# Kernel tuning notes

Measured on AMD Instinct MI355X. Metric: run time of the kernel, lower is better.

The kernel has to match this reference:

```python
import jax, jax.numpy as jnp
from jax import lax
import numpy as np

B, M, C, H, W = 32, 2, 256, 16, 16
N = H * W            # 256, square case required by the original bmm chain
DIM = 256            # hardcoded self.dim in the module
THR = 0.1
RATIO = 0.8


def conv2d(x, w, b):
    y = lax.conv_general_dilated(x, w, (1, 1), 'SAME',
                                 dimension_numbers=('NCHW', 'OIHW', 'NCHW'))
    return y + b[None, :, None, None]


def setup_inputs() -> dict:
    key = jax.random.key(0)
    ks = jax.random.split(key, 8)
    return {
        'con_feat': jax.random.normal(ks[0], (B, M, C, H, W), jnp.float32),
        'feat_s':   jax.random.normal(ks[1], (B, M, C, C), jnp.float32),
        'feat_v':   jax.random.uniform(ks[2], (B, M, C), jnp.float32),
        'feat_d':   jax.random.normal(ks[3], (B, M, N, N), jnp.float32),
        'w_enc':    jax.random.normal(ks[4], (C, C, 3, 3), jnp.float32) * 0.02,
        'b_enc':    jnp.zeros((C,), jnp.float32),
        'w_dec':    jax.random.normal(ks[5], (C, C, 3, 3), jnp.float32) * 0.02,
        'b_dec':    jnp.zeros((C,), jnp.float32),
        'w_val':    jax.random.normal(ks[6], (1, 2 * C, 3, 3), jnp.float32) * 0.02,
        'b_val':    jnp.zeros((1,), jnp.float32),
    }


def _assemble(fs, fv, fd, counts):
    # fs: (M,C,C) row blocks, fv: (M,C) diag values, fd: (M,N,N) col blocks, counts: (M,)
    big = max(C, N)                                  # out-of-range sentinel -> dropped
    off = jnp.cumsum(counts) - counts                # exclusive prefix offsets (M,)
    r = jnp.arange(C)
    dest = off[:, None] + r[None, :]                 # (M,C) destination slots
    valid = (r[None, :] < counts[:, None]) & (dest >= 0)
    dest = jnp.where(valid, dest, big).reshape(-1)   # (M*C,)
    ns = jnp.zeros((C, C), fs.dtype).at[dest].set(fs.reshape(M * C, C), mode='drop')
    fd_cols = fd[:, :, :C].transpose(0, 2, 1).reshape(M * C, N)  # source columns as rows
    ndT = jnp.zeros((N, N), fd.dtype).at[dest].set(fd_cols, mode='drop')
    nv = jnp.zeros((C, N), fv.dtype).at[dest, dest].set(fv.reshape(-1), mode='drop')
    return ns, nv, ndT.T


def reference(con_feat, feat_s, feat_v, feat_d, w_enc, b_enc, w_dec, b_dec, w_val, b_val):
    x = con_feat.reshape(B * M, C, H, W)
    # autoencoder reconstruction loss (training branch)
    mid = jax.nn.relu(conv2d(x, w_enc, b_enc))
    x_rec = conv2d(mid, w_dec, b_dec)
    auto_enc_loss = jnp.mean((x - x_rec) ** 2)

    # data-dependent rank budget per (batch, modality)
    counts = jnp.sum(feat_v > THR, axis=-1).astype(jnp.int32)      # (B,M)
    total = jnp.sum(counts, axis=-1)                               # (B,)
    kmin = min(C, N)
    adj = jnp.round(kmin * counts.astype(jnp.float32)
                    / jnp.maximum(total, 1)[:, None].astype(jnp.float32)).astype(jnp.int32)
    if M > 1:
        adj = adj.at[:, -1].set(DIM - jnp.sum(adj[:, :-1], axis=-1))
    counts = jnp.maximum(jnp.where((total > kmin)[:, None], adj, counts), 0)

    # scatter-assemble s/v/d and reconstruct
    ns, nv, nd = jax.vmap(_assemble)(feat_s, feat_v, feat_d, counts)
    rec = jnp.matmul(jnp.matmul(ns, nv), nd)                        # (B,C,N)
    rec = rec.reshape(B, C, H, W)
    rec = conv2d(rec, w_dec, b_dec)                                 # decoder
    rec = (rec - rec.min()) / (rec.max() - rec.min()) * 2.0 - 1.0

    # per-modality value scores, softmax over modality
    scores = jnp.stack([
        jax.nn.sigmoid(jax.nn.relu(conv2d(
            jnp.concatenate([rec, con_feat[:, m]], axis=1), w_val, b_val)))
        for m in range(M)
    ], axis=1)                                                      # (B,M,1,H,W)
    scores = jax.nn.softmax(scores, axis=1)
    fused = jnp.sum((1.0 - RATIO) * scores * con_feat, axis=1) + rec * RATIO
    return fused, auto_enc_loss
```

## Files before the change

kernel.cpp:

```cpp
#include <hip/hip_runtime.h>
#include <math.h>


typedef __attribute__((ext_vector_type(8))) short short8;
typedef __attribute__((ext_vector_type(4))) float f32x4;

__device__ __forceinline__ void gload_lds16(const void* g, void* l) {
  __builtin_amdgcn_global_load_lds(
      (const __attribute__((address_space(1))) void*)g,
      (__attribute__((address_space(3))) void*)l, 16, 0, 0);
}

__device__ __forceinline__ unsigned short f2bf(float f) {
  unsigned u = __float_as_uint(f);
  unsigned r = (u + 0x7FFFu + ((u >> 16) & 1u)) >> 16;
  return (unsigned short)r;
}

__device__ __forceinline__ unsigned mapf(float f) {
  unsigned u = __float_as_uint(f);
  return (u & 0x80000000u) ? ~u : (u | 0x80000000u);
}
__device__ __forceinline__ float unmapf(unsigned u) {
  unsigned v = (u & 0x80000000u) ? (u & 0x7fffffffu) : ~u;
  return __uint_as_float(v);
}

__global__ __launch_bounds__(256) void prep_k(
    const float* __restrict__ cf, const float* __restrict__ we,
    const float* __restrict__ wd, const float* __restrict__ fv,
    unsigned short* __restrict__ Xp, unsigned short* __restrict__ WrE,
    unsigned short* __restrict__ WrD, int* __restrict__ smr,
    float* __restrict__ vd, float4* __restrict__ sraw4,
    float* __restrict__ lacc, unsigned* __restrict__ mm) {
  const int bx = blockIdx.x, t = threadIdx.x;
  if (bx < 2048) {
    int idx = bx * 256 + t;
    int ch = idx & 31, p = (idx >> 5) & 255, img = idx >> 13;
    int ic0 = ch * 8;
    const float* sp = cf + (size_t)img * 65536 + (size_t)ic0 * 256 + p;
    unsigned short h[8];
#pragma unroll
    for (int i = 0; i < 8; ++i) h[i] = f2bf(sp[i * 256]);
    int y = p >> 4, x = p & 15;
    uint4 u;
    u.x = h[0] | (h[1] << 16); u.y = h[2] | (h[3] << 16);
    u.z = h[4] | (h[5] << 16); u.w = h[6] | (h[7] << 16);
    *(uint4*)&Xp[(size_t)img * 82944 + (size_t)(y * 18 + x + 19) * 256 + ic0] = u;
  } else if (bx < 2624) {
    int idx = (bx - 2048) * 256 + t;
    int ch = idx & 31, rest = idx >> 5;
    int s = rest % 9, ocx = rest / 9;
    int oc = ocx & 255, cv = ocx >> 8;
    const float* w = cv ? wd : we;
    unsigned short* o = cv ? WrD : WrE;
    int ic0 = ch * 8;
    unsigned short h[8];
#pragma unroll
    for (int i = 0; i < 8; ++i) h[i] = f2bf(w[(size_t)oc * 2304 + (ic0 + i) * 9 + s]);
    uint4 u;
    u.x = h[0] | (h[1] << 16); u.y = h[2] | (h[3] << 16);
    u.z = h[4] | (h[5] << 16); u.w = h[6] | (h[7] << 16);
    *(uint4*)&o[(size_t)oc * 2304 + s * 256 + ic0] = u;
  } else if (bx < 2752) {
    int img = bx - 2624;
    uint4* base = (uint4*)Xp + (size_t)img * 10368;
    uint4 z; z.x = z.y = z.z = z.w = 0;
    for (int it = t; it < 2176; it += 256) {
      int px = it >> 5, c = it & 31;
      int y, x;
      if (px < 18)      { y = 0;  x = px; }
      else if (px < 36) { y = 17; x = px - 18; }
      else if (px < 52) { y = px - 35; x = 0; }
      else              { y = px - 51; x = 17; }
      base[(y * 18 + x) * 32 + c] = z;
    }
  } else if (bx < 2784) {
    const int b = bx - 2752;
    const float v0 = fv[(size_t)b * 512 + t];
    const float v1 = fv[(size_t)b * 512 + 256 + t];
    const unsigned long long bal0 = __ballot(v0 > 0.1f);
    const unsigned long long bal1 = __ballot(v1 > 0.1f);
    __shared__ int cnt0[4], cnt1[4], fc[2];
    const int wid = t >> 6, lane = t & 63;
    if (lane == 0) { cnt0[wid] = __popcll(bal0); cnt1[wid] = __popcll(bal1); }
    smr[b * 256 + t] = -1;
    vd[b * 256 + t] = 0.f;
    __syncthreads();
    if (t == 0) {
      int c0 = cnt0[0] + cnt0[1] + cnt0[2] + cnt0[3];
      int c1 = cnt1[0] + cnt1[1] + cnt1[2] + cnt1[3];
      int total = c0 + c1;
      int f0, f1;
      if (total > 256) {
        int a0 = (int)rintf(256.0f * (float)c0 / (float)total);
        f0 = a0; f1 = 256 - a0;
      } else { f0 = c0; f1 = c1; }
      fc[0] = max(f0, 0); fc[1] = max(f1, 0);
    }
    __syncthreads();
    const int c0 = fc[0], c1 = fc[1];
    if (t < c0) { smr[b * 256 + t] = t; vd[b * 256 + t] = v0; }
    if (t < c1) {
      int d = c0 + t;
      if (d < 256) { smr[b * 256 + d] = 256 + t; vd[b * 256 + d] = v1; }
    }
  } else {
    int z = bx - 2784;
    if (z < 24) {
      float4 zz; zz.x = zz.y = zz.z = zz.w = 0.f;
      sraw4[z * 256 + t] = zz;
    } else if (t == 0) {
      lacc[0] = 0.f; mm[0] = 0xFFFFFFFFu; mm[1] = 0u;
    }
  }
}

template<int EPI, int IPSHIFT>
__global__ __launch_bounds__(256, 2) void convmma_k(
    const unsigned short* __restrict__ Xin, const unsigned short* __restrict__ Wr,
    const float* __restrict__ bias, const float* __restrict__ cfref,
    unsigned short* __restrict__ outp, float* __restrict__ outf,
    float* __restrict__ lacc, unsigned* __restrict__ mm) {
  __shared__ __align__(16) unsigned short S[3][12288];
  const int t = threadIdx.x, lane = t & 63, wave = t >> 6;
  const int L = blockIdx.x;
  const int xcd = L & 7, sl = L >> 3;
  const int img = xcd * (1 << IPSHIFT) + (sl & ((1 << IPSHIFT) - 1));
  const int tile = sl >> IPSHIFT;
  const int pt = tile >> 1, ot = tile & 1;

  int laneA[2], laneB[4];
  {
    const int rl = lane >> 3, q0 = lane & 7;
#pragma unroll
    for (int j = 0; j < 2; ++j) {
      int row = (wave * 2 + j) * 8 + rl;
      int p = pt * 64 + row, y = p >> 4, x = p & 15;
      laneA[j] = (y * 18 + x) * 512 + ((q0 ^ (row & 7)) * 16);
    }
#pragma unroll
    for (int j = 0; j < 4; ++j) {
      int row = (wave * 4 + j) * 8 + rl;
      laneB[j] = (ot * 128 + row) * 4608 + ((q0 ^ (row & 7)) * 16);
    }
  }
  const char* Ag = (const char*)Xin + (size_t)img * 165888;
  const char* Bg = (const char*)Wr;

  const int mlane = lane & 15, quad = lane >> 4;
  const int mw = wave >> 1, nw = wave & 1;
  int aoff[2][2], boff[4][2];
#pragma unroll
  for (int ks = 0; ks < 2; ++ks) {
#pragma unroll
    for (int i = 0; i < 2; ++i) {
      int rowm = mw * 32 + i * 16 + mlane;
      aoff[i][ks] = rowm * 128 + (((ks * 4 + quad) ^ (rowm & 7)) * 16);
    }
#pragma unroll
    for (int n = 0; n < 4; ++n) {
      int rown = nw * 64 + n * 16 + mlane;
      boff[n][ks] = 8192 + rown * 128 + (((ks * 4 + quad) ^ (rown & 7)) * 16);
    }
  }

  auto stage = [&](int kit, int buf) {
    int s = kit >> 2;
    int dy = s / 3, dx = s - dy * 3;
    int aG = (dy * 18 + dx) * 512 + (kit & 3) * 128;
    int bG = kit * 128;
    char* dst = (char*)S[buf];
#pragma unroll
    for (int j = 0; j < 2; ++j)
      gload_lds16(Ag + laneA[j] + aG, dst + (wave * 2 + j) * 1024);
#pragma unroll
    for (int j = 0; j < 4; ++j)
      gload_lds16(Bg + laneB[j] + bG, dst + 8192 + (wave * 4 + j) * 1024);
  };

  f32x4 acc[2][4] = {};
  auto compute = [&](int buf) {
    const char* Sb = (const char*)S[buf];
#pragma unroll
    for (int ks = 0; ks < 2; ++ks) {
      short8 af[2], bf[4];
#pragma unroll
      for (int i = 0; i < 2; ++i) af[i] = *(const short8*)(Sb + aoff[i][ks]);
#pragma unroll
      for (int n = 0; n < 4; ++n) bf[n] = *(const short8*)(Sb + boff[n][ks]);
#pragma unroll
      for (int i = 0; i < 2; ++i)
#pragma unroll
        for (int n = 0; n < 4; ++n)
          acc[i][n] = __builtin_amdgcn_mfma_f32_16x16x32_bf16(af[i], bf[n], acc[i][n], 0, 0, 0);
    }
  };

  stage(0, 0);
  stage(1, 1);
  int cur = 0, nxt = 2;
  for (int kit = 0; kit < 35; ++kit) {
    asm volatile("s_waitcnt vmcnt(6)" ::: "memory");
    asm volatile("s_barrier" ::: "memory");
    if (kit + 2 < 36) stage(kit + 2, nxt);
    compute(cur);
    cur = (cur == 2) ? 0 : cur + 1;
    nxt = (nxt == 2) ? 0 : nxt + 1;
  }
  asm volatile("s_waitcnt vmcnt(0)" ::: "memory");
  asm volatile("s_barrier" ::: "memory");
  compute(cur);

  if (EPI == 0) {
#pragma unroll
    for (int i = 0; i < 2; ++i) {
      int m0 = pt * 64 + mw * 32 + i * 16 + quad * 4;
#pragma unroll
      for (int n = 0; n < 4; ++n) {
        int oc = ot * 128 + nw * 64 + n * 16 + mlane;
        float bv = bias[oc];
#pragma unroll
        for (int r = 0; r < 4; ++r) {
          int p = m0 + r;
          int y = p >> 4, x = p & 15;
          float v = fmaxf(acc[i][n][r] + bv, 0.f);
          outp[(size_t)img * 82944 + (size_t)(y * 18 + x + 19) * 256 + oc] = f2bf(v);
        }
      }
    }
  } else if (EPI == 1) {
    float ls = 0.f;
#pragma unroll
    for (int i = 0; i < 2; ++i) {
      int m0 = pt * 64 + mw * 32 + i * 16 + quad * 4;
#pragma unroll
      for (int n = 0; n < 4; ++n) {
        int oc = ot * 128 + nw * 64 + n * 16 + mlane;
        float bv = bias[oc];
        float4 c4 = *(const float4*)(cfref + (size_t)img * 65536 + (size_t)oc * 256 + m0);
        float d0 = acc[i][n][0] + bv - c4.x;
        float d1 = acc[i][n][1] + bv - c4.y;
        float d2 = acc[i][n][2] + bv - c4.z;
        float d3 = acc[i][n][3] + bv - c4.w;
        ls += d0 * d0 + d1 * d1 + d2 * d2 + d3 * d3;
      }
    }
#pragma unroll
    for (int off = 32; off; off >>= 1) ls += __shfl_down(ls, off);
    __shared__ float sred[4];
    if (lane == 0) sred[wave] = ls;
    __syncthreads();
    if (t == 0) atomicAdd(lacc, sred[0] + sred[1] + sred[2] + sred[3]);
  } else {
    float mn = INFINITY, mx = -INFINITY;
#pragma unroll
    for (int i = 0; i < 2; ++i) {
      int m0 = pt * 64 + mw * 32 + i * 16 + quad * 4;
#pragma unroll
      for (int n = 0; n < 4; ++n) {
        int oc = ot * 128 + nw * 64 + n * 16 + mlane;
        float bv = bias[oc];
        float4 v;
        v.x = acc[i][n][0] + bv; v.y = acc[i][n][1] + bv;
        v.z = acc[i][n][2] + bv; v.w = acc[i][n][3] + bv;
        mn = fminf(mn, fminf(fminf(v.x, v.y), fminf(v.z, v.w)));
        mx = fmaxf(mx, fmaxf(fmaxf(v.x, v.y), fmaxf(v.z, v.w)));
        *(float4*)(outf + (size_t)img * 65536 + (size_t)oc * 256 + m0) = v;
      }
    }
#pragma unroll
    for (int off = 32; off; off >>= 1) {
      mn = fminf(mn, __shfl_down(mn, off));
      mx = fmaxf(mx, __shfl_down(mx, off));
    }
    __shared__ float smn[4], smx[4];
    if (lane == 0) { smn[wave] = mn; smx[wave] = mx; }
    __syncthreads();
    if (t == 0) {
      mn = fminf(fminf(smn[0], smn[1]), fminf(smn[2], smn[3]));
      mx = fmaxf(fmaxf(smx[0], smx[1]), fmaxf(smx[2], smx[3]));
      atomicMin(&mm[0], mapf(mn));
      atomicMax(&mm[1], mapf(mx));
    }
  }
}

__global__ __launch_bounds__(256) void ansbmt_k(
    const float* __restrict__ fs, const float* __restrict__ fd,
    const int* __restrict__ smr, const float* __restrict__ vd,
    unsigned short* __restrict__ Ans, unsigned short* __restrict__ BmT,
    unsigned short* __restrict__ Recp) {
  const int bx = blockIdx.x, t = threadIdx.x;
  if (bx < 1024) {
    int idx = bx * 256 + t;
    int ch = idx & 31, c = (idx >> 5) & 255, b = idx >> 13;
    int j0 = ch * 8;
    int si = smr[b * 256 + c];
    unsigned short h[8] = {0, 0, 0, 0, 0, 0, 0, 0};
    if (si >= 0) {
      int m = si >> 8, r = si & 255;
      const float* fp = fs + (((size_t)b * 2 + m) * 256 + r) * 256 + j0;
      const float* vp = vd + b * 256 + j0;
#pragma unroll
      for (int i = 0; i < 8; ++i) h[i] = f2bf(fp[i] * vp[i]);
    }
    uint4 u;
    u.x = h[0] | (h[1] << 16); u.y = h[2] | (h[3] << 16);
    u.z = h[4] | (h[5] << 16); u.w = h[6] | (h[7] << 16);
    *(uint4*)&Ans[(size_t)b * 65536 + c * 256 + j0] = u;
  } else if (bx < 1152) {
    __shared__ float sIn[4096];
    const int b = (bx - 1024) >> 2, bz = (bx - 1024) & 3;
    const int sp = smr[b * 256 + t];
    const int m_p = sp >> 8, r_p = sp & 255;
    for (int jg = bz * 8; jg < bz * 8 + 8; ++jg) {
      __syncthreads();
#pragma unroll
      for (int u = 0; u < 4; ++u) {
        int q = t * 4 + u;
        int rr = q >> 6, w = q & 63;
        int m = rr >> 3, i = rr & 7;
        float4 f = ((const float4*)fd)[((size_t)(b * 2 + m) * 256 + jg * 8 + i) * 64 + w];
        *(float4*)&sIn[i * 512 + m * 256 + w * 4] = f;
      }
      __syncthreads();
      unsigned short h[8] = {0, 0, 0, 0, 0, 0, 0, 0};
      if (sp >= 0) {
#pragma unroll
        for (int i = 0; i < 8; ++i) h[i] = f2bf(sIn[i * 512 + m_p * 256 + r_p]);
      }
      uint4 u;
      u.x = h[0] | (h[1] << 16); u.y = h[2] | (h[3] << 16);
      u.z = h[4] | (h[5] << 16); u.w = h[6] | (h[7] << 16);
      *(uint4*)&BmT[(size_t)b * 65536 + t * 256 + jg * 8] = u;
    }
  } else {
    int img = bx - 1152;
    uint4* base = (uint4*)Recp + (size_t)img * 10368;
    uint4 z; z.x = z.y = z.z = z.w = 0;
    for (int it = t; it < 2176; it += 256) {
      int px = it >> 5, c = it & 31;
      int y, x;
      if (px < 18)      { y = 0;  x = px; }
      else if (px < 36) { y = 17; x = px - 18; }
      else if (px < 52) { y = px - 35; x = 0; }
      else              { y = px - 51; x = 17; }
      base[(y * 18 + x) * 32 + c] = z;
    }
  }
}

__global__ __launch_bounds__(256, 4) void recgemm_k(const unsigned short* __restrict__ BmT,
                                                    const unsigned short* __restrict__ Ans,
                                                    unsigned short* __restrict__ Recp) {
  __shared__ __align__(16) unsigned short S[2][8192];
  const int t = threadIdx.x, lane = t & 63, wave = t >> 6;
  const int b = blockIdx.y, pt = blockIdx.x >> 2, ct = blockIdx.x & 3;

  int laneA[2], laneB[2];
#pragma unroll
  for (int j = 0; j < 2; ++j) {
    int id = (wave * 2 + j) * 64 + lane;
    int row = id >> 3, q = (id & 7) ^ (row & 7);
    laneA[j] = (pt * 64 + row) * 512 + q * 16;
    laneB[j] = (ct * 64 + row) * 512 + q * 16;
  }
  const char* Ag = (const char*)BmT + (size_t)b * 131072;
  const char* Bg = (const char*)Ans + (size_t)b * 131072;

  const int mlane = lane & 15, quad = lane >> 4;
  const int mw = wave >> 1, nw = wave & 1;
  int aoff[2][2], boff[2][2];
#pragma unroll
  for (int ks = 0; ks < 2; ++ks) {
#pragma unroll
    for (int i = 0; i < 2; ++i) {
      int rowm = mw * 32 + i * 16 + mlane;
      aoff[i][ks] = rowm * 128 + (((ks * 4 + quad) ^ (rowm & 7)) * 16);
      int rown = nw * 32 + i * 16 + mlane;
      boff[i][ks] = 8192 + rown * 128 + (((ks * 4 + quad) ^ (rown & 7)) * 16);
    }
  }

  auto stage = [&](int kit, int buf) {
    int g = kit * 128;
    char* dst = (char*)S[buf];
#pragma unroll
    for (int j = 0; j < 2; ++j)
      gload_lds16(Ag + laneA[j] + g, dst + (wave * 2 + j) * 1024);
#pragma unroll
    for (int j = 0; j < 2; ++j)
      gload_lds16(Bg + laneB[j] + g, dst + 8192 + (wave * 2 + j) * 1024);
  };

  f32x4 acc[2][2] = {};
  stage(0, 0);
  for (int kit = 0; kit < 4; ++kit) {
    int cur = kit & 1;
    asm volatile("s_waitcnt vmcnt(0)" ::: "memory");
    asm volatile("s_barrier" ::: "memory");
    if (kit + 1 < 4) stage(kit + 1, 1 - cur);
    const char* Sb = (const char*)S[cur];
#pragma unroll
    for (int ks = 0; ks < 2; ++ks) {
      short8 af[2], bf[2];
#pragma unroll
      for (int i = 0; i < 2; ++i) {
        af[i] = *(const short8*)(Sb + aoff[i][ks]);
        bf[i] = *(const short8*)(Sb + boff[i][ks]);
      }
#pragma unroll
      for (int i = 0; i < 2; ++i)
#pragma unroll
        for (int n = 0; n < 2; ++n)
          acc[i][n] = __builtin_amdgcn_mfma_f32_16x16x32_bf16(af[i], bf[n], acc[i][n], 0, 0, 0);
    }
  }

#pragma unroll
  for (int i = 0; i < 2; ++i) {
    int m0 = pt * 64 + mw * 32 + i * 16 + quad * 4;
#pragma unroll
    for (int n = 0; n < 2; ++n) {
      int cc = ct * 64 + nw * 32 + n * 16 + mlane;
#pragma unroll
      for (int r = 0; r < 4; ++r) {
        int p = m0 + r;
        int y = p >> 4, x = p & 15;
        Recp[(size_t)b * 82944 + (size_t)(y * 18 + x + 19) * 256 + cc] = f2bf(acc[i][n][r]);
      }
    }
  }
}

__global__ __launch_bounds__(256) void score_conv_k(
    const float* __restrict__ rec2, const float* __restrict__ cf,
    const float* __restrict__ wval, const unsigned* __restrict__ mm,
    float* __restrict__ sraw) {
  const int b = blockIdx.x, phase = blockIdx.y, icc = blockIdx.z;
  const int t = threadIdx.x;
  const int row = t >> 4, col = t & 15;
  __shared__ float s_in[8 * 360];
  __shared__ float s_wv[72];
  for (int i = t; i < 8 * 360; i += 256) s_in[i] = 0.f;
  const float* src;
  float sc = 1.f, sh = 0.f;
  int wofs;
  if (phase == 0) {
    src = rec2 + (size_t)b * 65536;
    float mn = unmapf(mm[0]), mx = unmapf(mm[1]);
    sc = 2.f / (mx - mn);
    sh = -mn * sc - 1.f;
    wofs = 0;
  } else {
    src = cf + ((size_t)b * 2 + (phase - 1)) * 65536;
    wofs = 2304;
  }
  float acc = 0.f;
  for (int ic0 = icc * 32; ic0 < icc * 32 + 32; ic0 += 8) {
    __syncthreads();
#pragma unroll
    for (int i = 0; i < 8; ++i) {
      float v = src[(ic0 + i) * 256 + t];
      if (phase == 0) v = fmaf(v, sc, sh);
      s_in[i * 360 + (row + 1) * 20 + (col + 1)] = v;
    }
    if (t < 72) s_wv[t] = wval[wofs + ic0 * 9 + t];
    __syncthreads();
#pragma unroll
    for (int i = 0; i < 8; ++i)
#pragma unroll
      for (int ky = 0; ky < 3; ++ky)
#pragma unroll
        for (int kx = 0; kx < 3; ++kx)
          acc += s_in[i * 360 + (row + ky) * 20 + (col + kx)] * s_wv[i * 9 + ky * 3 + kx];
  }
  atomicAdd(&sraw[((size_t)b * 3 + phase) * 256 + t], acc);
}

__global__ void fuse_k(const float* __restrict__ cf, const float* __restrict__ rec2,
                       const float* __restrict__ sraw, const float* __restrict__ bval,
                       const unsigned* __restrict__ mm, const float* __restrict__ lacc,
                       float* __restrict__ outp) {
  const int idx = blockIdx.x * 256 + threadIdx.x;
  const int b = idx >> 16;
  const int rest = idx & 65535;
  const int pos = idx & 255;
  const float mn = unmapf(mm[0]), mx = unmapf(mm[1]);
  const float sc = 2.f / (mx - mn), sh = -mn * sc - 1.f;
  const float srec = sraw[(size_t)b * 768 + pos];
  const float sc0 = sraw[(size_t)b * 768 + 256 + pos];
  const float sc1 = sraw[(size_t)b * 768 + 512 + pos];
  const float bv = bval[0];
  const float z0 = fmaxf(srec + sc0 + bv, 0.f);
  const float z1 = fmaxf(srec + sc1 + bv, 0.f);
  const float s0 = 1.f / (1.f + expf(-z0));
  const float s1 = 1.f / (1.f + expf(-z1));
  const float w0 = 1.f / (1.f + expf(s1 - s0));
  const float w1 = 1.f - w0;
  const float rn = fmaf(rec2[idx], sc, sh);
  const float f0 = cf[(size_t)b * 131072 + rest];
  const float f1 = cf[(size_t)b * 131072 + 65536 + rest];
  outp[idx] = 0.2f * (w0 * f0 + w1 * f1) + 0.8f * rn;
  if (idx == 0) outp[2097152] = lacc[0] * (1.f / 4194304.f);
}

extern "C" void kernel_launch(void* const* d_in, const int* in_sizes, int n_in,
                              void* d_out, int out_size, void* d_ws, size_t ws_size,
                              hipStream_t stream) {
  const float* cf    = (const float*)d_in[0];
  const float* fs    = (const float*)d_in[1];
  const float* fv    = (const float*)d_in[2];
  const float* fd    = (const float*)d_in[3];
  const float* w_enc = (const float*)d_in[4];
  const float* b_enc = (const float*)d_in[5];
  const float* w_dec = (const float*)d_in[6];
  const float* b_dec = (const float*)d_in[7];
  const float* w_val = (const float*)d_in[8];
  const float* b_val = (const float*)d_in[9];
  float* out = (float*)d_out;
  float* wsf = (float*)d_ws;

  unsigned short* Xp   = (unsigned short*)wsf;
  unsigned short* Ans  = (unsigned short*)wsf;
  unsigned short* BmT  = (unsigned short*)(wsf + 1048576);
  unsigned short* Midp = (unsigned short*)(wsf + 2654208);
  unsigned short* Recp = (unsigned short*)(wsf + 2654208);
  float* rec2 = wsf + 5308416;
  unsigned short* WrE = (unsigned short*)(wsf + 7405568);
  unsigned short* WrD = (unsigned short*)(wsf + 7700480);
  float* sraw = wsf + 7995392;
  float* vd   = wsf + 8019968;
  int*   smr  = (int*)(wsf + 8028160);
  float* lacc = wsf + 8036352;
  unsigned* mm = (unsigned*)(wsf + 8036354);

  prep_k<<<2809, 256, 0, stream>>>(cf, w_enc, w_dec, fv, Xp, WrE, WrD, smr, vd,
                                   (float4*)sraw, lacc, mm);
  convmma_k<0, 3><<<512, 256, 0, stream>>>(Xp, WrE, b_enc, nullptr, Midp, nullptr, nullptr, nullptr);
  convmma_k<1, 3><<<512, 256, 0, stream>>>(Midp, WrD, b_dec, cf, nullptr, nullptr, lacc, nullptr);
  ansbmt_k<<<1184, 256, 0, stream>>>(fs, fd, smr, vd, Ans, BmT, Recp);
  recgemm_k<<<dim3(16, 32), 256, 0, stream>>>(BmT, Ans, Recp);
  convmma_k<2, 2><<<256, 256, 0, stream>>>(Recp, WrD, b_dec, nullptr, nullptr, rec2, nullptr, mm);
  score_conv_k<<<dim3(32, 3, 8), 256, 0, stream>>>(rec2, cf, w_val, mm, sraw);
  fuse_k<<<8192, 256, 0, stream>>>(cf, rec2, sraw, b_val, mm, lacc, out);
}
```

Baseline: 242.9 us.

## Merge decoder convs into one launch with larger 128x128 tiles

Replaces the templated conv kernel with separate encoder and decoder kernels that use 512-thread blocks and 128-pixel tiles, with double buffering instead of triple buffering. The loss-decoder conv and the reconstruction-decoder conv now run in a single launch over 96 image units, which needs a reordered workspace so Recp no longer aliases Midp. The assembly and reconstruction GEMMs are moved before the encoder conv. The prep transpose index order is also changed so that global reads are coalesced along pixels. The aim is fewer launches and better weight reuse per block. The cost is that the loop now waits on vmcnt(0) every iteration, which reduces load/compute overlap.

Result: faster. 215.8 us (-11.2%).

```diff
diff --git a/kernel.cpp b/kernel.cpp
--- a/kernel.cpp
+++ b/kernel.cpp
@@ -36,7 +36,7 @@
   const int bx = blockIdx.x, t = threadIdx.x;
   if (bx < 2048) {
     int idx = bx * 256 + t;
-    int ch = idx & 31, p = (idx >> 5) & 255, img = idx >> 13;
+    int p = idx & 255, ch = (idx >> 8) & 31, img = idx >> 13;
     int ic0 = ch * 8;
     const float* sp = cf + (size_t)img * 65536 + (size_t)ic0 * 256 + p;
     unsigned short h[8];
@@ -116,34 +116,26 @@
   }
 }
 
-template<int EPI, int IPSHIFT>
-__global__ __launch_bounds__(256, 2) void convmma_k(
+
+__global__ __launch_bounds__(512, 4) void conv_enc_k(
     const unsigned short* __restrict__ Xin, const unsigned short* __restrict__ Wr,
-    const float* __restrict__ bias, const float* __restrict__ cfref,
-    unsigned short* __restrict__ outp, float* __restrict__ outf,
-    float* __restrict__ lacc, unsigned* __restrict__ mm) {
-  __shared__ __align__(16) unsigned short S[3][12288];
+    const float* __restrict__ bias, unsigned short* __restrict__ outp) {
+  __shared__ __align__(16) char S[2][32768];
   const int t = threadIdx.x, lane = t & 63, wave = t >> 6;
   const int L = blockIdx.x;
   const int xcd = L & 7, sl = L >> 3;
-  const int img = xcd * (1 << IPSHIFT) + (sl & ((1 << IPSHIFT) - 1));
-  const int tile = sl >> IPSHIFT;
+  const int img = xcd * 8 + (sl & 7);
+  const int tile = sl >> 3;
   const int pt = tile >> 1, ot = tile & 1;
 
-  int laneA[2], laneB[4];
-  {
-    const int rl = lane >> 3, q0 = lane & 7;
-#pragma unroll
-    for (int j = 0; j < 2; ++j) {
-      int row = (wave * 2 + j) * 8 + rl;
-      int p = pt * 64 + row, y = p >> 4, x = p & 15;
-      laneA[j] = (y * 18 + x) * 512 + ((q0 ^ (row & 7)) * 16);
-    }
-#pragma unroll
-    for (int j = 0; j < 4; ++j) {
-      int row = (wave * 4 + j) * 8 + rl;
-      laneB[j] = (ot * 128 + row) * 4608 + ((q0 ^ (row & 7)) * 16);
-    }
+  int laneA[2], laneB[2];
+#pragma unroll
+  for (int r = 0; r < 2; ++r) {
+    int id = r * 512 + t;
+    int row = id >> 3, sub = id & 7, q = sub ^ (row & 7);
+    int p = pt * 128 + row, y = p >> 4, x = p & 15;
+    laneA[r] = (y * 18 + x) * 512 + q * 16;
+    laneB[r] = (ot * 128 + row) * 4608 + q * 16;
   }
   const char* Ag = (const char*)Xin + (size_t)img * 165888;
   const char* Bg = (const char*)Wr;
@@ -161,7 +153,7 @@
 #pragma unroll
     for (int n = 0; n < 4; ++n) {
       int rown = nw * 64 + n * 16 + mlane;
-      boff[n][ks] = 8192 + rown * 128 + (((ks * 4 + quad) ^ (rown & 7)) * 16);
+      boff[n][ks] = 16384 + rown * 128 + (((ks * 4 + quad) ^ (rown & 7)) * 16);
     }
   }
 
@@ -170,18 +162,18 @@
     int dy = s / 3, dx = s - dy * 3;
     int aG = (dy * 18 + dx) * 512 + (kit & 3) * 128;
     int bG = kit * 128;
-    char* dst = (char*)S[buf];
-#pragma unroll
-    for (int j = 0; j < 2; ++j)
-      gload_lds16(Ag + laneA[j] + aG, dst + (wave * 2 + j) * 1024);
-#pragma unroll
-    for (int j = 0; j < 4; ++j)
-      gload_lds16(Bg + laneB[j] + bG, dst + 8192 + (wave * 4 + j) * 1024);
+    char* dst = S[buf];
+#pragma unroll
+    for (int r = 0; r < 2; ++r)
+      gload_lds16(Ag + laneA[r] + aG, dst + r * 8192 + wave * 1024);
+#pragma unroll
+    for (int r = 0; r < 2; ++r)
+      gload_lds16(Bg + laneB[r] + bG, dst + 16384 + r * 8192 + wave * 1024);
   };
 
   f32x4 acc[2][4] = {};
   auto compute = [&](int buf) {
-    const char* Sb = (const char*)S[buf];
+    const char* Sb = S[buf];
 #pragma unroll
     for (int ks = 0; ks < 2; ++ks) {
       short8 af[2], bf[4];
@@ -198,47 +190,127 @@
   };
 
   stage(0, 0);
-  stage(1, 1);
-  int cur = 0, nxt = 2;
-  for (int kit = 0; kit < 35; ++kit) {
-    asm volatile("s_waitcnt vmcnt(6)" ::: "memory");
+  for (int kit = 0; kit < 36; ++kit) {
+    int cur = kit & 1;
+    asm volatile("s_waitcnt vmcnt(0)" ::: "memory");
     asm volatile("s_barrier" ::: "memory");
-    if (kit + 2 < 36) stage(kit + 2, nxt);
+    if (kit + 1 < 36) stage(kit + 1, 1 - cur);
     compute(cur);
-    cur = (cur == 2) ? 0 : cur + 1;
-    nxt = (nxt == 2) ? 0 : nxt + 1;
-  }
-  asm volatile("s_waitcnt vmcnt(0)" ::: "memory");
-  asm volatile("s_barrier" ::: "memory");
-  compute(cur);
-
-  if (EPI == 0) {
+  }
+
+#pragma unroll
+  for (int i = 0; i < 2; ++i) {
+    int m0 = pt * 128 + mw * 32 + i * 16 + quad * 4;
+#pragma unroll
+    for (int n = 0; n < 4; ++n) {
+      int oc = ot * 128 + nw * 64 + n * 16 + mlane;
+      float bv = bias[oc];
+#pragma unroll
+      for (int r = 0; r < 4; ++r) {
+        int p = m0 + r;
+        int y = p >> 4, x = p & 15;
+        float v = fmaxf(acc[i][n][r] + bv, 0.f);
+        outp[(size_t)img * 82944 + (size_t)(y * 18 + x + 19) * 256 + oc] = f2bf(v);
+      }
+    }
+  }
+}
+
+__global__ __launch_bounds__(512, 4) void conv_dec_k(
+    const unsigned short* __restrict__ Midp, const unsigned short* __restrict__ Recp,
+    const unsigned short* __restrict__ Wr, const float* __restrict__ bias,
+    const float* __restrict__ cfref, float* __restrict__ rec2,
+    float* __restrict__ lacc, unsigned* __restrict__ mm) {
+  __shared__ __align__(16) char S[2][32768];
+  const int t = threadIdx.x, lane = t & 63, wave = t >> 6;
+  const int L = blockIdx.x;
+  const int xcd = L & 7, sl = L >> 3;
+  const int u12 = sl % 12, tile = sl / 12;
+  const int unit = xcd * 12 + u12;
+  const bool isLoss = unit < 64;
+  const int pt = tile >> 1, ot = tile & 1;
+
+  int laneA[2], laneB[2];
+#pragma unroll
+  for (int r = 0; r < 2; ++r) {
+    int id = r * 512 + t;
+    int row = id >> 3, sub = id & 7, q = sub ^ (row & 7);
+    int p = pt * 128 + row, y = p >> 4, x = p & 15;
+    laneA[r] = (y * 18 + x) * 512 + q * 16;
+    laneB[r] = (ot * 128 + row) * 4608 + q * 16;
+  }
+  const char* Ag = isLoss ? (const char*)Midp + (size_t)unit * 165888
+                          : (const char*)Recp + (size_t)(unit - 64) * 165888;
+  const char* Bg = (const char*)Wr;
+
+  const int mlane = lane & 15, quad = lane >> 4;
+  const int mw = wave >> 1, nw = wave & 1;
+  int aoff[2][2], boff[4][2];
+#pragma unroll
+  for (int ks = 0; ks < 2; ++ks) {
 #pragma unroll
     for (int i = 0; i < 2; ++i) {
-      int m0 = pt * 64 + mw * 32 + i * 16 + quad * 4;
+      int rowm = mw * 32 + i * 16 + mlane;
+      aoff[i][ks] = rowm * 128 + (((ks * 4 + quad) ^ (rowm & 7)) * 16);
+    }
+#pragma unroll
+    for (int n = 0; n < 4; ++n) {
+      int rown = nw * 64 + n * 16 + mlane;
+      boff[n][ks] = 16384 + rown * 128 + (((ks * 4 + quad) ^ (rown & 7)) * 16);
+    }
+  }
+
+  auto stage = [&](int kit, int buf) {
+    int s = kit >> 2;
+    int dy = s / 3, dx = s - dy * 3;
+    int aG = (dy * 18 + dx) * 512 + (kit & 3) * 128;
+    int bG = kit * 128;
+    char* dst = S[buf];
+#pragma unroll
+    for (int r = 0; r < 2; ++r)
+      gload_lds16(Ag + laneA[r] + aG, dst + r * 8192 + wave * 1024);
+#pragma unroll
+    for (int r = 0; r < 2; ++r)
+      gload_lds16(Bg + laneB[r] + bG, dst + 16384 + r * 8192 + wave * 1024);
+  };
+
+  f32x4 acc[2][4] = {};
+  auto compute = [&](int buf) {
+    const char* Sb = S[buf];
+#pragma unroll
+    for (int ks = 0; ks < 2; ++ks) {
+      short8 af[2], bf[4];
+#pragma unroll
+      for (int i = 0; i < 2; ++i) af[i] = *(const short8*)(Sb + aoff[i][ks]);
+#pragma unroll
+      for (int n = 0; n < 4; ++n) bf[n] = *(const short8*)(Sb + boff[n][ks]);
+#pragma unroll
+      for (int i = 0; i < 2; ++i)
+#pragma unroll
+        for (int n = 0; n < 4; ++n)
+          acc[i][n] = __builtin_amdgcn_mfma_f32_16x16x32_bf16(af[i], bf[n], acc[i][n], 0, 0, 0);
+    }
+  };
+
+  stage(0, 0);
+  for (int kit = 0; kit < 36; ++kit) {
+    int cur = kit & 1;
+    asm volatile("s_waitcnt vmcnt(0)" ::: "memory");
+    asm volatile("s_barrier" ::: "memory");
+    if (kit + 1 < 36) stage(kit + 1, 1 - cur);
+    compute(cur);
+  }
+
+  if (isLoss) {
+    float ls = 0.f;
+#pragma unroll
+    for (int i = 0; i < 2; ++i) {
+      int m0 = pt * 128 + mw * 32 + i * 16 + quad * 4;
 #pragma unroll
       for (int n = 0; n < 4; ++n) {
         int oc = ot * 128 + nw * 64 + n * 16 + mlane;
         float bv = bias[oc];
-#pragma unroll
-        for (int r = 0; r < 4; ++r) {
-          int p = m0 + r;
-          int y = p >> 4, x = p & 15;
-          float v = fmaxf(acc[i][n][r] + bv, 0.f);
-          outp[(size_t)img * 82944 + (size_t)(y * 18 + x + 19) * 256 + oc] = f2bf(v);
-        }
-      }
-    }
-  } else if (EPI == 1) {
-    float ls = 0.f;
-#pragma unroll
-    for (int i = 0; i < 2; ++i) {
-      int m0 = pt * 64 + mw * 32 + i * 16 + quad * 4;
-#pragma unroll
-      for (int n = 0; n < 4; ++n) {
-        int oc = ot * 128 + nw * 64 + n * 16 + mlane;
-        float bv = bias[oc];
-        float4 c4 = *(const float4*)(cfref + (size_t)img * 65536 + (size_t)oc * 256 + m0);
+        float4 c4 = *(const float4*)(cfref + (size_t)unit * 65536 + (size_t)oc * 256 + m0);
         float d0 = acc[i][n][0] + bv - c4.x;
         float d1 = acc[i][n][1] + bv - c4.y;
         float d2 = acc[i][n][2] + bv - c4.z;
@@ -248,15 +320,21 @@
     }
 #pragma unroll
     for (int off = 32; off; off >>= 1) ls += __shfl_down(ls, off);
-    __shared__ float sred[4];
+    __shared__ float sred[8];
     if (lane == 0) sred[wave] = ls;
     __syncthreads();
-    if (t == 0) atomicAdd(lacc, sred[0] + sred[1] + sred[2] + sred[3]);
+    if (t == 0) {
+      float s = 0.f;
+#pragma unroll
+      for (int w = 0; w < 8; ++w) s += sred[w];
+      atomicAdd(lacc, s);
+    }
   } else {
+    const int img2 = unit - 64;
     float mn = INFINITY, mx = -INFINITY;
 #pragma unroll
     for (int i = 0; i < 2; ++i) {
-      int m0 = pt * 64 + mw * 32 + i * 16 + quad * 4;
+      int m0 = pt * 128 + mw * 32 + i * 16 + quad * 4;
 #pragma unroll
       for (int n = 0; n < 4; ++n) {
         int oc = ot * 128 + nw * 64 + n * 16 + mlane;
@@ -266,7 +344,7 @@
         v.z = acc[i][n][2] + bv; v.w = acc[i][n][3] + bv;
         mn = fminf(mn, fminf(fminf(v.x, v.y), fminf(v.z, v.w)));
         mx = fmaxf(mx, fmaxf(fmaxf(v.x, v.y), fmaxf(v.z, v.w)));
-        *(float4*)(outf + (size_t)img * 65536 + (size_t)oc * 256 + m0) = v;
+        *(float4*)(rec2 + (size_t)img2 * 65536 + (size_t)oc * 256 + m0) = v;
       }
     }
 #pragma unroll
@@ -274,14 +352,15 @@
       mn = fminf(mn, __shfl_down(mn, off));
       mx = fmaxf(mx, __shfl_down(mx, off));
     }
-    __shared__ float smn[4], smx[4];
+    __shared__ float smn[8], smx[8];
     if (lane == 0) { smn[wave] = mn; smx[wave] = mx; }
     __syncthreads();
     if (t == 0) {
-      mn = fminf(fminf(smn[0], smn[1]), fminf(smn[2], smn[3]));
-      mx = fmaxf(fmaxf(smx[0], smx[1]), fmaxf(smx[2], smx[3]));
-      atomicMin(&mm[0], mapf(mn));
-      atomicMax(&mm[1], mapf(mx));
+      float a = INFINITY, b2 = -INFINITY;
+#pragma unroll
+      for (int w = 0; w < 8; ++w) { a = fminf(a, smn[w]); b2 = fmaxf(b2, smx[w]); }
+      atomicMin(&mm[0], mapf(a));
+      atomicMax(&mm[1], mapf(b2));
     }
   }
 }
@@ -523,26 +602,25 @@
   float* wsf = (float*)d_ws;
 
   unsigned short* Xp   = (unsigned short*)wsf;
-  unsigned short* Ans  = (unsigned short*)wsf;
-  unsigned short* BmT  = (unsigned short*)(wsf + 1048576);
   unsigned short* Midp = (unsigned short*)(wsf + 2654208);
-  unsigned short* Recp = (unsigned short*)(wsf + 2654208);
-  float* rec2 = wsf + 5308416;
-  unsigned short* WrE = (unsigned short*)(wsf + 7405568);
-  unsigned short* WrD = (unsigned short*)(wsf + 7700480);
-  float* sraw = wsf + 7995392;
-  float* vd   = wsf + 8019968;
-  int*   smr  = (int*)(wsf + 8028160);
-  float* lacc = wsf + 8036352;
-  unsigned* mm = (unsigned*)(wsf + 8036354);
+  unsigned short* Recp = (unsigned short*)(wsf + 5308416);
+  float* rec2 = wsf + 6635520;
+  unsigned short* WrE = (unsigned short*)(wsf + 8732672);
+  unsigned short* WrD = (unsigned short*)(wsf + 9027584);
+  unsigned short* Ans = (unsigned short*)(wsf + 9322496);
+  unsigned short* BmT = (unsigned short*)(wsf + 10371072);
+  float* sraw = wsf + 11419648;
+  float* vd   = wsf + 11444224;
+  int*   smr  = (int*)(wsf + 11452416);
+  float* lacc = wsf + 11460608;
+  unsigned* mm = (unsigned*)(wsf + 11460609);
 
   prep_k<<<2809, 256, 0, stream>>>(cf, w_enc, w_dec, fv, Xp, WrE, WrD, smr, vd,
                                    (float4*)sraw, lacc, mm);
-  convmma_k<0, 3><<<512, 256, 0, stream>>>(Xp, WrE, b_enc, nullptr, Midp, nullptr, nullptr, nullptr);
-  convmma_k<1, 3><<<512, 256, 0, stream>>>(Midp, WrD, b_dec, cf, nullptr, nullptr, lacc, nullptr);
   ansbmt_k<<<1184, 256, 0, stream>>>(fs, fd, smr, vd, Ans, BmT, Recp);
   recgemm_k<<<dim3(16, 32), 256, 0, stream>>>(BmT, Ans, Recp);
-  convmma_k<2, 2><<<256, 256, 0, stream>>>(Recp, WrD, b_dec, nullptr, nullptr, rec2, nullptr, mm);
+  conv_enc_k<<<256, 512, 0, stream>>>(Xp, WrE, b_enc, Midp);
+  conv_dec_k<<<384, 512, 0, stream>>>(Midp, Recp, WrD, b_dec, cf, rec2, lacc, mm);
   score_conv_k<<<dim3(32, 3, 8), 256, 0, stream>>>(rec2, cf, w_val, mm, sraw);
   fuse_k<<<8192, 256, 0, stream>>>(cf, rec2, sraw, b_val, mm, lacc, out);
 }
```
